# Performance work log

Hardware: AMD Instinct MI355X
Metric: run time of the kernel (lower is better)

## Reference

```python
import jax, jax.numpy as jnp
import numpy as np

SQRT_2_OVER_PI = 0.7978845608028654

def gelu_tanh(x):
    return 0.5 * x * (1.0 + jnp.tanh(SQRT_2_OVER_PI * (x + 0.044715 * x ** 3)))

def setup_inputs() -> dict:
    key = jax.random.key(0)
    ks = jax.random.split(key, 16)
    B, L, H, Dk, Dv = 4, 512, 8, 64, 64
    dm = H * Dk
    inp = {
        'q': jax.random.normal(ks[0], (B, L, dm), jnp.float32),
        'k': jax.random.normal(ks[1], (B, L, dm), jnp.float32),
        'v': jax.random.normal(ks[2], (B, L, dm), jnp.float32),
        'vec_adj_k': jax.random.normal(ks[3], (B, L, L, Dk), jnp.float32),
        'vec_adj_v': jax.random.normal(ks[4], (B, L, L, Dv), jnp.float32),
        'adj_k': jax.random.randint(ks[5], (B, L, L), 0, 2, jnp.int32),
        'adj_v': jax.random.randint(ks[6], (B, L, L), 0, 2, jnp.int32),
        # learned params (Linear weights stored as [in, out]; y = x @ W)
        'w_qs': jax.random.normal(ks[7], (dm, H * Dk), jnp.float32) * 0.02,
        'w_ks': jax.random.normal(ks[8], (dm, H * Dk), jnp.float32) * 0.02,
        'w_vs': jax.random.normal(ks[9], (dm, H * Dv), jnp.float32) * 0.02,
        'w_fc': jax.random.normal(ks[10], (H * Dk, H * Dk), jnp.float32) * 0.02,
        'w_nw': jax.random.normal(ks[11], (H * Dk, 1), jnp.float32) * 0.02,
        'w_self': jax.random.normal(ks[12], (H * Dk, H * Dk), jnp.float32) * 0.02,
        'w_dd': jax.random.normal(ks[13], (H * Dk, H * Dk), jnp.float32) * 0.02,
    }
    return inp

def reference(q, k, v, vec_adj_k, vec_adj_v, adj_k, adj_v,
              w_qs, w_ks, w_vs, w_fc, w_nw, w_self, w_dd):
    H, Dk, Dv = 8, 64, 64
    B, L, dm = q.shape
    temperature = Dk ** 0.5
    residual = q
    # projections -> [B, H, L, D]
    qh = (q @ w_qs).reshape(B, L, H, Dk).transpose(0, 2, 1, 3)
    kh = (k @ w_ks).reshape(B, L, H, Dk).transpose(0, 2, 1, 3)
    vh = (v @ w_vs).reshape(B, L, H, Dv).transpose(0, 2, 1, 3)
    qs = qh / temperature
    # inner_(q, k, vec_adj_k, flag=True): content + relative-position scores
    scores = jnp.einsum('bhld,bhmd->bhlm', qs, kh) \
           + jnp.einsum('bhld,blmd->bhlm', qs, vec_adj_k)  # [B,H,L,L]
    # adjacency mask (mask == 0 -> -10000)
    scores = jnp.where(adj_k[:, None, :, :] == 0, jnp.float32(-10000.0), scores)
    attn = jax.nn.softmax(scores, axis=-1)
    # inner_(attn, v, vec_adj_v, flag=False)
    out = jnp.einsum('bhlm,bhmd->bhld', attn, vh) \
        + jnp.einsum('bhlm,blmd->bhld', attn, vec_adj_v)
    qc = out.transpose(0, 2, 1, 3).reshape(B, L, H * Dv)  # [B,L,dm]
    # masked neighbor aggregation (GNN stage)
    adj_f = adj_k.astype(qc.dtype)
    nn_num = adj_f.sum(-1)                                  # [B,L]
    denom = jnp.where(nn_num >= 1.0, nn_num, 1.0)
    node_weight = jax.nn.sigmoid((qc @ w_nw)[..., 0])       # [B,L]
    self_info = qc @ w_self
    dd_info = qc @ w_dd
    dd_weight = node_weight[:, None, :] * adj_f             # [B,L,L]
    agg = jnp.matmul(dd_weight, dd_info) / denom[..., None]
    qo = gelu_tanh((self_info + agg) @ w_fc)
    qo = residual + qo
    return (qo, attn)
```

## Files before the change

kernel.cpp:

```cpp
#include <hip/hip_runtime.h>
#include <cstdint>


typedef __attribute__((ext_vector_type(8))) short short8;
typedef __attribute__((ext_vector_type(4))) float f32x4;

__device__ __forceinline__ unsigned short f2bf(float f){
  union { float f; unsigned u; } v; v.f = f;
  unsigned r = (v.u + 0x7fffu + ((v.u >> 16) & 1u)) >> 16;
  return (unsigned short)r;
}

__device__ __forceinline__ short8 ld8(const unsigned short* p){
  return *(const short8*)p;
}

__device__ __forceinline__ f32x4 mfma16(short8 a, short8 b, f32x4 c){
  return __builtin_amdgcn_mfma_f32_16x16x32_bf16(a, b, c, 0, 0, 0);
}

__device__ __forceinline__ float gelu_tanh(float x){
  float u = 0.7978845608028654f * (x + 0.044715f * x * x * x);
  return 0.5f * x * (1.f + tanhf(u));
}

__device__ __forceinline__ short8 pack8(float4 f0, float4 f1){
  short8 s;
  s[0] = (short)f2bf(f0.x); s[1] = (short)f2bf(f0.y);
  s[2] = (short)f2bf(f0.z); s[3] = (short)f2bf(f0.w);
  s[4] = (short)f2bf(f1.x); s[5] = (short)f2bf(f1.y);
  s[6] = (short)f2bf(f1.z); s[7] = (short)f2bf(f1.w);
  return s;
}

template<int MT, int LDA, int LDB, int KSTEPS>
__device__ __forceinline__ void gemmT(const unsigned short* __restrict__ A,
                                      const unsigned short* __restrict__ Bp,
                                      f32x4 acc[MT][4]){
#pragma unroll 2
  for (int ks = 0; ks < KSTEPS; ks++){
    int kk = ks * 32;
    short8 a[MT], b[4];
#pragma unroll
    for (int i = 0; i < MT; i++) a[i] = ld8(A + (size_t)i * 16 * LDA + kk);
#pragma unroll
    for (int j = 0; j < 4; j++)  b[j] = ld8(Bp + (size_t)j * 16 * LDB + kk);
#pragma unroll
    for (int i = 0; i < MT; i++)
#pragma unroll
      for (int j = 0; j < 4; j++)
        acc[i][j] = mfma16(a[i], b[j], acc[i][j]);
  }
}

__global__ __launch_bounds__(256) void k_prep(const float* __restrict__ q,
    const float* __restrict__ k, const float* __restrict__ v,
    unsigned short* __restrict__ xin,
    const float* __restrict__ wqs, const float* __restrict__ wks,
    const float* __restrict__ wvs, const float* __restrict__ wself,
    const float* __restrict__ wdd, const float* __restrict__ wfc,
    unsigned short* __restrict__ Wt){
  int blk = blockIdx.x;
  int t = threadIdx.x;
  if (blk < 3072){
    int i = blk * 256 + t;
    int w = i >> 18, r = i & 262143;
    const float* src = (w == 0) ? q : (w == 1) ? k : v;
    float4 f = *(const float4*)(src + (size_t)r * 4);
    unsigned lo = (unsigned)f2bf(f.x) | ((unsigned)f2bf(f.y) << 16);
    unsigned hi = (unsigned)f2bf(f.z) | ((unsigned)f2bf(f.w) << 16);
    uint2 o; o.x = lo; o.y = hi;
    *(uint2*)(xin + (size_t)w * 1048576 + (size_t)r * 4) = o;
  } else {
    int i = (blk - 3072) * 256 + t;
    int w = i >> 13;
    int rr = i & 8191;
    int kg = rr >> 9;
    int n  = rr & 511;
    int k0 = kg * 32;
    const float* src = (w == 0) ? wqs : (w == 1) ? wks : (w == 2) ? wvs :
                       (w == 3) ? wself : (w == 4) ? wdd : wfc;
    unsigned pk[16];
#pragma unroll
    for (int j = 0; j < 16; j++){
      float a = src[(size_t)(k0 + 2 * j) * 512 + n];
      float b = src[(size_t)(k0 + 2 * j + 1) * 512 + n];
      pk[j] = (unsigned)f2bf(a) | ((unsigned)f2bf(b) << 16);
    }
    uint4* o4 = (uint4*)(Wt + (size_t)w * 262144 + (size_t)n * 512 + k0);
    o4[0] = make_uint4(pk[0],  pk[1],  pk[2],  pk[3]);
    o4[1] = make_uint4(pk[4],  pk[5],  pk[6],  pk[7]);
    o4[2] = make_uint4(pk[8],  pk[9],  pk[10], pk[11]);
    o4[3] = make_uint4(pk[12], pk[13], pk[14], pk[15]);
  }
}

__global__ __launch_bounds__(256) void k_proj(const unsigned short* __restrict__ xin,
    const unsigned short* __restrict__ Wt, unsigned short* __restrict__ qsb,
    unsigned short* __restrict__ khb, unsigned short* __restrict__ vhT){
  int wid = blockIdx.x * 4 + (threadIdx.x >> 6);
  int mode = wid >> 9;
  int tile = wid & 511;
  int tm = tile >> 3, tn = tile & 7;
  int lane = threadIdx.x & 63;
  int r = lane & 15, qq = lane >> 4;
  const unsigned short* X = xin + (size_t)mode * 1048576;
  const unsigned short* W = Wt + (size_t)mode * 262144;
  unsigned short* dst = (mode == 0) ? qsb : (mode == 1) ? khb : vhT;
  const unsigned short* A  = X + (size_t)(tm * 32 + r) * 512 + qq * 8;
  const unsigned short* Bp = W + (size_t)(tn * 64 + r) * 512 + qq * 8;
  f32x4 acc[2][4] = {};
  gemmT<2, 512, 512, 16>(A, Bp, acc);
  float scv = (mode == 0) ? 0.125f : 1.0f;
  int h = tn;
#pragma unroll
  for (int i = 0; i < 2; i++)
#pragma unroll
    for (int j = 0; j < 4; j++)
#pragma unroll
      for (int e = 0; e < 4; e++){
        int row = tm * 32 + i * 16 + qq * 4 + e;
        int d = j * 16 + r;
        int bb = row >> 9, l = row & 511;
        unsigned short val = f2bf(acc[i][j][e] * scv);
        size_t idx = (mode == 2) ? ((size_t)((bb * 8 + h) * 64 + d) * 512 + l)
                                 : ((size_t)((bb * 8 + h) * 512 + l) * 64 + d);
        dst[idx] = val;
      }
}

__global__ __launch_bounds__(256) void k_scores(const unsigned short* __restrict__ qs,
    const unsigned short* __restrict__ kh, float* __restrict__ attnF){
  int wid = blockIdx.x * 4 + (threadIdx.x >> 6);
  int bh = wid >> 6;
  int tile = wid & 63;
  int tm = tile >> 3, tn = tile & 7;
  int lane = threadIdx.x & 63;
  int r = lane & 15, qq = lane >> 4;
  const unsigned short* A  = qs + (size_t)bh * 32768 + (size_t)(tm * 64 + r) * 64 + qq * 8;
  const unsigned short* Bp = kh + (size_t)bh * 32768 + (size_t)(tn * 64 + r) * 64 + qq * 8;
  f32x4 acc[4][4] = {};
  gemmT<4, 64, 64, 2>(A, Bp, acc);
  float* C = attnF + (size_t)bh * 262144;
#pragma unroll
  for (int i = 0; i < 4; i++)
#pragma unroll
    for (int j = 0; j < 4; j++)
#pragma unroll
      for (int e = 0; e < 4; e++){
        int row = tm * 64 + i * 16 + qq * 4 + e;
        int col = tn * 64 + j * 16 + r;
        C[(size_t)row * 512 + col] = acc[i][j][e];
      }
}

__global__ __launch_bounds__(256) void k_relsoft(const unsigned short* __restrict__ qs,
    const float* __restrict__ vak, const int* __restrict__ adj,
    float* __restrict__ attnF, unsigned short* __restrict__ attn_bf){
  int bid = blockIdx.x;
  int b = bid >> 9, l = bid & 511;
  int t = threadIdx.x, lane = t & 63, w = t >> 6;
  __shared__ __align__(16) unsigned short qsA[16 * 64];
  __shared__ float sc[8 * 512];
  __shared__ short Mlist[512];
  __shared__ int lds4[4];
  for (int j = 0; j < 4; j++){
    int e = t + j * 256;
    int m = e >> 6, d = e & 63;
    qsA[e] = (m < 8) ? qs[((size_t)((b * 8 + m) * 512 + l)) * 64 + d] : (unsigned short)0;
  }
  int am0 = adj[(size_t)bid * 512 + t];
  int am1 = adj[(size_t)bid * 512 + t + 256];
  for (int j = 0; j < 16; j++){
    int e = t + j * 256;
    int h = e >> 9, m = e & 511;
    float s = attnF[((size_t)(b * 8 + h) * 512 + l) * 512 + m];
    int msk = (j & 1) ? am1 : am0;
    sc[e] = msk ? s : -10000.0f;
  }
  int2 av2 = *(const int2*)(adj + (size_t)bid * 512 + 2 * t);
  int c = av2.x + av2.y;
  int incl = c;
  for (int off = 1; off < 64; off <<= 1){
    int n = __shfl_up(incl, off, 64);
    if (lane >= off) incl += n;
  }
  if (lane == 63) lds4[w] = incl;
  __syncthreads();
  int base = 0;
  for (int i = 0; i < w; i++) base += lds4[i];
  int cnt = lds4[0] + lds4[1] + lds4[2] + lds4[3];
  int excl = base + incl - c;
  if (av2.x){ Mlist[excl] = (short)(2 * t); excl++; }
  if (av2.y){ Mlist[excl] = (short)(2 * t + 1); }
  int padded = (cnt + 31) & ~31;
  for (int i2 = cnt + t; i2 < padded; i2 += 256) Mlist[i2] = 0;
  __syncthreads();
  int r = lane & 15, qq = lane >> 4;
  short8 a0 = ld8(qsA + r * 64 + qq * 8);
  short8 a1 = ld8(qsA + r * 64 + 32 + qq * 8);
  const float* vrow = vak + (size_t)bid * 32768;
  int ntiles = (cnt + 15) >> 4;
  for (int tile = w; tile < ntiles; tile += 4){
    int gi = tile * 16 + r;
    int m = Mlist[gi];
    const float* p = vrow + (size_t)m * 64 + qq * 8;
    float4 f0 = *(const float4*)(p);
    float4 f1 = *(const float4*)(p + 4);
    float4 f2 = *(const float4*)(p + 32);
    float4 f3 = *(const float4*)(p + 36);
    f32x4 acc = {0.f, 0.f, 0.f, 0.f};
    acc = mfma16(a0, pack8(f0, f1), acc);
    acc = mfma16(a1, pack8(f2, f3), acc);
    if (qq < 2){
#pragma unroll
      for (int i = 0; i < 4; i++){
        int h = qq * 4 + i;
        if (gi < cnt) sc[h * 512 + m] += acc[i];
      }
    }
  }
  __syncthreads();
  for (int hh = 0; hh < 2; hh++){
    int h = w * 2 + hh;
    float v[8]; float mx = -3.0e38f;
    for (int i = 0; i < 8; i++){
      int m = lane + i * 64;
      v[i] = sc[h * 512 + m]; mx = fmaxf(mx, v[i]);
    }
    for (int off = 32; off; off >>= 1) mx = fmaxf(mx, __shfl_xor(mx, off, 64));
    float sum = 0.f;
    for (int i = 0; i < 8; i++){ v[i] = __expf(v[i] - mx); sum += v[i]; }
    for (int off = 32; off; off >>= 1) sum += __shfl_xor(sum, off, 64);
    float inv = 1.f / sum;
    size_t base2 = ((size_t)(b * 8 + h) * 512 + l) * 512;
    for (int i = 0; i < 8; i++){
      int m = lane + i * 64;
      float p2 = v[i] * inv;
      attnF[base2 + m] = p2;
      attn_bf[base2 + m] = f2bf(p2);
    }
  }
}

__global__ __launch_bounds__(256) void k_outc(const unsigned short* __restrict__ attn_bf,
    const unsigned short* __restrict__ vhT, float* __restrict__ qc){
  int wid = blockIdx.x * 4 + (threadIdx.x >> 6);
  int bh = wid >> 4;
  int tm = wid & 15;
  int lane = threadIdx.x & 63;
  int r = lane & 15, qq = lane >> 4;
  const unsigned short* A  = attn_bf + (size_t)bh * 262144 + (size_t)(tm * 32 + r) * 512 + qq * 8;
  const unsigned short* Bp = vhT + (size_t)bh * 32768 + (size_t)r * 512 + qq * 8;
  f32x4 acc[2][4] = {};
  gemmT<2, 512, 512, 16>(A, Bp, acc);
  int b = bh >> 3, h = bh & 7;
#pragma unroll
  for (int i = 0; i < 2; i++)
#pragma unroll
    for (int j = 0; j < 4; j++)
#pragma unroll
      for (int e = 0; e < 4; e++){
        int lrow = tm * 32 + i * 16 + qq * 4 + e;
        int d = j * 16 + r;
        qc[(size_t)(b * 512 + lrow) * 512 + h * 64 + d] = acc[i][j][e];
      }
}

__global__ __launch_bounds__(256) void k_outrel(const unsigned short* __restrict__ attn_bf,
    const float* __restrict__ vav, const float* __restrict__ qc,
    const int* __restrict__ adj, const float* __restrict__ wnw,
    unsigned short* __restrict__ qc_bf, float* __restrict__ nw, float* __restrict__ invden){
  int bid = blockIdx.x;
  int b = bid >> 9, l = bid & 511;
  int t = threadIdx.x, lane = t & 63, w = t >> 6;
  __shared__ __align__(16) unsigned short attnL[8][512];
  __shared__ __align__(16) unsigned short pAg[8][528];
  __shared__ short Mlist[512];
  __shared__ float orL[512];
  __shared__ float redf[4];
  __shared__ int lds4[4];
  int r = lane & 15, qq = lane >> 4;
  int h8 = r & 7;
#pragma unroll
  for (int h = 0; h < 8; h++){
    const unsigned short* rowp = attn_bf + (((size_t)(b * 8 + h) * 512 + l) * 512);
    *(ushort2*)(&attnL[h][2 * t]) = *(const ushort2*)(rowp + 2 * t);
  }
  int2 av2 = *(const int2*)(adj + (size_t)bid * 512 + 2 * t);
  int c = av2.x + av2.y;
  int incl = c;
  for (int off = 1; off < 64; off <<= 1){
    int n = __shfl_up(incl, off, 64);
    if (lane >= off) incl += n;
  }
  if (lane == 63) lds4[w] = incl;
  __syncthreads();
  int base = 0;
  for (int i = 0; i < w; i++) base += lds4[i];
  int cnt = lds4[0] + lds4[1] + lds4[2] + lds4[3];
  int excl = base + incl - c;
  if (av2.x){ Mlist[excl] = (short)(2 * t); excl++; }
  if (av2.y){ Mlist[excl] = (short)(2 * t + 1); }
  int cntV = cnt;
  int padded0 = (cnt + 31) & ~31;
  for (int i2 = cnt + t; i2 < padded0; i2 += 256) Mlist[i2] = 0;
  __syncthreads();
  if (cnt == 0){
    for (int i2 = t; i2 < 512; i2 += 256) Mlist[i2] = (short)i2;
    cntV = 512;
    __syncthreads();
  }
  int padded = (cntV + 31) & ~31;
  for (int j = t; j < padded; j += 256){
    int m = Mlist[j];
    bool vld = (j < cntV);
#pragma unroll
    for (int h = 0; h < 8; h++)
      pAg[h][j] = vld ? attnL[h][m] : (unsigned short)0;
  }
  __syncthreads();
  const float* vrow = vav + (size_t)bid * 32768;
  int dcol = w * 16 + r;
  f32x4 acc = {0.f, 0.f, 0.f, 0.f};
  int nks = padded >> 5;
  for (int s = 0; s < nks; s++){
    short8 av = ld8(&pAg[h8][s * 32 + qq * 8]);
    int mrow[8];
#pragma unroll
    for (int j = 0; j < 8; j++) mrow[j] = Mlist[s * 32 + qq * 8 + j];
    float fv[8];
#pragma unroll
    for (int j = 0; j < 8; j++) fv[j] = vrow[(size_t)mrow[j] * 64 + dcol];
    short8 bv;
#pragma unroll
    for (int j = 0; j < 8; j++) bv[j] = (short)f2bf(fv[j]);
    acc = mfma16(av, bv, acc);
  }
  if (qq < 2){
#pragma unroll
    for (int i = 0; i < 4; i++){
      int h = qq * 4 + i;
      orL[h * 64 + dcol] = acc[i];
    }
  }
  __syncthreads();
  float part = 0.f;
  for (int j = 0; j < 2; j++){
    int e = t + j * 256;
    float val = qc[(size_t)bid * 512 + e] + orL[e];
    qc_bf[(size_t)bid * 512 + e] = f2bf(val);
    part += val * wnw[e];
  }
  for (int off = 32; off; off >>= 1) part += __shfl_xor(part, off, 64);
  if (lane == 0) redf[w] = part;
  __syncthreads();
  if (t == 0){
    float tot = redf[0] + redf[1] + redf[2] + redf[3];
    nw[bid] = 1.f / (1.f + __expf(-tot));
    invden[bid] = 1.f / ((cnt >= 1) ? (float)cnt : 1.f);
  }
}

__global__ __launch_bounds__(256) void k_post(const unsigned short* __restrict__ qcb,
    const unsigned short* __restrict__ Wself, const unsigned short* __restrict__ Wdd,
    float* __restrict__ selfi, unsigned short* __restrict__ ddT,
    const int* __restrict__ adj, const float* __restrict__ nw,
    const float* __restrict__ invden, unsigned short* __restrict__ ddw){
  int blk = blockIdx.x;
  int t = threadIdx.x;
  if (blk < 256){
    int mode = blk >> 7;
    int wid = (blk & 127) * 4 + (t >> 6);
    int tm = wid >> 3, tn = wid & 7;
    int lane = t & 63;
    int r = lane & 15, qq = lane >> 4;
    const unsigned short* W = mode ? Wdd : Wself;
    const unsigned short* A  = qcb + (size_t)(tm * 32 + r) * 512 + qq * 8;
    const unsigned short* Bp = W + (size_t)(tn * 64 + r) * 512 + qq * 8;
    f32x4 acc[2][4] = {};
    gemmT<2, 512, 512, 16>(A, Bp, acc);
#pragma unroll
    for (int i = 0; i < 2; i++)
#pragma unroll
      for (int j = 0; j < 4; j++)
#pragma unroll
        for (int e = 0; e < 4; e++){
          int row = tm * 32 + i * 16 + qq * 4 + e;
          int col = tn * 64 + j * 16 + r;
          if (mode == 0)
            selfi[(size_t)row * 512 + col] = acc[i][j][e];
          else {
            int bb = row >> 9, m = row & 511;
            ddT[((size_t)(bb * 512 + col)) * 512 + m] = f2bf(acc[i][j][e]);
          }
        }
  } else {
    int i8 = ((blk - 256) * 256 + t) * 8;
    int bb = i8 >> 18, rest = i8 & 262143;
    int l = rest >> 9, m0 = rest & 511;
    int4 a0 = *(const int4*)(adj + i8);
    int4 a1 = *(const int4*)(adj + i8 + 4);
    float id = invden[bb * 512 + l];
    const float* nwb = nw + bb * 512 + m0;
    short8 o;
    o[0] = a0.x ? (short)f2bf(nwb[0] * id) : (short)0;
    o[1] = a0.y ? (short)f2bf(nwb[1] * id) : (short)0;
    o[2] = a0.z ? (short)f2bf(nwb[2] * id) : (short)0;
    o[3] = a0.w ? (short)f2bf(nwb[3] * id) : (short)0;
    o[4] = a1.x ? (short)f2bf(nwb[4] * id) : (short)0;
    o[5] = a1.y ? (short)f2bf(nwb[5] * id) : (short)0;
    o[6] = a1.z ? (short)f2bf(nwb[6] * id) : (short)0;
    o[7] = a1.w ? (short)f2bf(nwb[7] * id) : (short)0;
    *(short8*)(ddw + i8) = o;
  }
}

__global__ __launch_bounds__(256) void k_agg(const unsigned short* __restrict__ ddw,
    const unsigned short* __restrict__ ddT, const float* __restrict__ selfi,
    unsigned short* __restrict__ xbf){
  int wid = blockIdx.x * 4 + (threadIdx.x >> 6);
  int b = wid >> 7;
  int tile = wid & 127;
  int tm = tile >> 3, tn = tile & 7;
  int lane = threadIdx.x & 63;
  int r = lane & 15, qq = lane >> 4;
  const unsigned short* A  = ddw + (size_t)b * 262144 + (size_t)(tm * 32 + r) * 512 + qq * 8;
  const unsigned short* Bp = ddT + (size_t)b * 262144 + (size_t)(tn * 64 + r) * 512 + qq * 8;
  f32x4 acc[2][4] = {};
  gemmT<2, 512, 512, 16>(A, Bp, acc);
#pragma unroll
  for (int i = 0; i < 2; i++)
#pragma unroll
    for (int j = 0; j < 4; j++)
#pragma unroll
      for (int e = 0; e < 4; e++){
        int row = b * 512 + tm * 32 + i * 16 + qq * 4 + e;
        int col = tn * 64 + j * 16 + r;
        float x = acc[i][j][e] + selfi[(size_t)row * 512 + col];
        xbf[(size_t)row * 512 + col] = f2bf(x);
      }
}

__global__ __launch_bounds__(256) void k_fc(const unsigned short* __restrict__ xbf,
    const unsigned short* __restrict__ W, const float* __restrict__ qin,
    float* __restrict__ qo){
  int wid = blockIdx.x * 4 + (threadIdx.x >> 6);
  int tm = wid >> 3, tn = wid & 7;
  int lane = threadIdx.x & 63;
  int r = lane & 15, qq = lane >> 4;
  const unsigned short* A  = xbf + (size_t)(tm * 32 + r) * 512 + qq * 8;
  const unsigned short* Bp = W + (size_t)(tn * 64 + r) * 512 + qq * 8;
  f32x4 acc[2][4] = {};
  gemmT<2, 512, 512, 16>(A, Bp, acc);
#pragma unroll
  for (int i = 0; i < 2; i++)
#pragma unroll
    for (int j = 0; j < 4; j++)
#pragma unroll
      for (int e = 0; e < 4; e++){
        int row = tm * 32 + i * 16 + qq * 4 + e;
        int col = tn * 64 + j * 16 + r;
        qo[(size_t)row * 512 + col] = qin[(size_t)row * 512 + col] + gelu_tanh(acc[i][j][e]);
      }
}

extern "C" void kernel_launch(void* const* d_in, const int* in_sizes, int n_in,
                              void* d_out, int out_size, void* d_ws, size_t ws_size,
                              hipStream_t stream){
  const float* q    = (const float*)d_in[0];
  const float* k    = (const float*)d_in[1];
  const float* v    = (const float*)d_in[2];
  const float* vak  = (const float*)d_in[3];
  const float* vav  = (const float*)d_in[4];
  const int*   adjk = (const int*)d_in[5];
  const float* wqs  = (const float*)d_in[7];
  const float* wks  = (const float*)d_in[8];
  const float* wvs  = (const float*)d_in[9];
  const float* wfc  = (const float*)d_in[10];
  const float* wnw  = (const float*)d_in[11];
  const float* wself= (const float*)d_in[12];
  const float* wdd  = (const float*)d_in[13];

  float* qo    = (float*)d_out;
  float* attnF = qo + 1048576;

  char* p = (char*)d_ws;
  unsigned short* xin   = (unsigned short*)p; p += 6291456;
  unsigned short* Wt    = (unsigned short*)p; p += 3145728;
  unsigned short* qsb   = (unsigned short*)p; p += 2097152;
  unsigned short* khb   = (unsigned short*)p; p += 2097152;
  unsigned short* vhT   = (unsigned short*)p; p += 2097152;
  unsigned short* attnb = (unsigned short*)p; p += 16777216;
  float*          qc    = (float*)p;          p += 4194304;
  unsigned short* qcb   = (unsigned short*)p; p += 2097152;
  float*          nw    = (float*)p;          p += 8192;
  float*          invd  = (float*)p;          p += 8192;
  float*          selfi = (float*)p;          p += 4194304;
  unsigned short* ddT   = (unsigned short*)p; p += 2097152;
  unsigned short* ddw   = (unsigned short*)p; p += 2097152;
  unsigned short* xbf   = (unsigned short*)p; p += 2097152;

  k_prep<<<3264, 256, 0, stream>>>(q, k, v, xin, wqs, wks, wvs, wself, wdd, wfc, Wt);
  k_proj<<<384, 256, 0, stream>>>(xin, Wt, qsb, khb, vhT);
  k_scores<<<512, 256, 0, stream>>>(qsb, khb, attnF);
  k_relsoft<<<2048, 256, 0, stream>>>(qsb, vak, adjk, attnF, attnb);
  k_outc<<<128, 256, 0, stream>>>(attnb, vhT, qc);
  k_outrel<<<2048, 256, 0, stream>>>(attnb, vav, qc, adjk, wnw, qcb, nw, invd);
  k_post<<<768, 256, 0, stream>>>(qcb, Wt + 786432, Wt + 1048576, selfi, ddT,
                                  adjk, nw, invd, ddw);
  k_agg<<<128, 256, 0, stream>>>(ddw, ddT, selfi, xbf);
  k_fc<<<128, 256, 0, stream>>>(xbf, Wt + 1310720, q, qo);
}
```

Before: 618.9 us.

## Stage gathered relative-position vectors through LDS for coalesced loads in attention kernels

In k_relsoft, each wave now cooperatively loads the 16 gathered vec_adj_k rows of a tile with float4 loads, converts them to bf16 into a per-wave LDS buffer, and feeds the MFMA from LDS. In k_outrel, the per-lane scattered scalar loads of vec_adj_v are replaced by chunks of 128 gathered rows loaded block-wide as float4, transposed into LDS as bf16, then consumed by four MFMAs per chunk. The goal is to coalesce the dominant global traffic on the large vec_adj tensors. The cost is extra LDS space, block-level barriers per chunk, and padding to 128 rows, which adds wasted work when neighbour counts are small.

```diff
diff --git a/kernel.cpp b/kernel.cpp
--- a/kernel.cpp
+++ b/kernel.cpp
@@ -22,15 +22,6 @@
 __device__ __forceinline__ float gelu_tanh(float x){
   float u = 0.7978845608028654f * (x + 0.044715f * x * x * x);
   return 0.5f * x * (1.f + tanhf(u));
-}
-
-__device__ __forceinline__ short8 pack8(float4 f0, float4 f1){
-  short8 s;
-  s[0] = (short)f2bf(f0.x); s[1] = (short)f2bf(f0.y);
-  s[2] = (short)f2bf(f0.z); s[3] = (short)f2bf(f0.w);
-  s[4] = (short)f2bf(f1.x); s[5] = (short)f2bf(f1.y);
-  s[6] = (short)f2bf(f1.z); s[7] = (short)f2bf(f1.w);
-  return s;
 }
 
 template<int MT, int LDA, int LDB, int KSTEPS>
@@ -161,6 +152,7 @@
   int b = bid >> 9, l = bid & 511;
   int t = threadIdx.x, lane = t & 63, w = t >> 6;
   __shared__ __align__(16) unsigned short qsA[16 * 64];
+  __shared__ __align__(16) unsigned short vkt[4][16 * 72];
   __shared__ float sc[8 * 512];
   __shared__ short Mlist[512];
   __shared__ int lds4[4];
@@ -201,17 +193,25 @@
   short8 a1 = ld8(qsA + r * 64 + 32 + qq * 8);
   const float* vrow = vak + (size_t)bid * 32768;
   int ntiles = (cnt + 15) >> 4;
+  unsigned short* vw = &vkt[w][0];
   for (int tile = w; tile < ntiles; tile += 4){
-    int gi = tile * 16 + r;
+    int rows0 = tile * 16;
+#pragma unroll
+    for (int it = 0; it < 4; it++){
+      int idx = it * 64 + lane;
+      int rloc = idx >> 4, seg = idx & 15;
+      int ms = Mlist[rows0 + rloc];
+      float4 f = *(const float4*)(vrow + (size_t)ms * 64 + seg * 4);
+      ushort4 u;
+      u.x = f2bf(f.x); u.y = f2bf(f.y); u.z = f2bf(f.z); u.w = f2bf(f.w);
+      *(ushort4*)(vw + rloc * 72 + seg * 4) = u;
+    }
+    int gi = rows0 + r;
     int m = Mlist[gi];
-    const float* p = vrow + (size_t)m * 64 + qq * 8;
-    float4 f0 = *(const float4*)(p);
-    float4 f1 = *(const float4*)(p + 4);
-    float4 f2 = *(const float4*)(p + 32);
-    float4 f3 = *(const float4*)(p + 36);
+    const unsigned short* bp = vw + r * 72 + qq * 8;
     f32x4 acc = {0.f, 0.f, 0.f, 0.f};
-    acc = mfma16(a0, pack8(f0, f1), acc);
-    acc = mfma16(a1, pack8(f2, f3), acc);
+    acc = mfma16(a0, ld8(bp),      acc);
+    acc = mfma16(a1, ld8(bp + 32), acc);
     if (qq < 2){
 #pragma unroll
       for (int i = 0; i < 4; i++){
@@ -275,7 +275,8 @@
   int b = bid >> 9, l = bid & 511;
   int t = threadIdx.x, lane = t & 63, w = t >> 6;
   __shared__ __align__(16) unsigned short attnL[8][512];
-  __shared__ __align__(16) unsigned short pAg[8][528];
+  __shared__ __align__(16) unsigned short pAg[8][512];
+  __shared__ __align__(16) unsigned short vvT[64 * 136];
   __shared__ short Mlist[512];
   __shared__ float orL[512];
   __shared__ float redf[4];
@@ -303,15 +304,15 @@
   if (av2.x){ Mlist[excl] = (short)(2 * t); excl++; }
   if (av2.y){ Mlist[excl] = (short)(2 * t + 1); }
   int cntV = cnt;
-  int padded0 = (cnt + 31) & ~31;
-  for (int i2 = cnt + t; i2 < padded0; i2 += 256) Mlist[i2] = 0;
   __syncthreads();
   if (cnt == 0){
     for (int i2 = t; i2 < 512; i2 += 256) Mlist[i2] = (short)i2;
     cntV = 512;
     __syncthreads();
   }
-  int padded = (cntV + 31) & ~31;
+  int padded = (cntV + 127) & ~127;
+  for (int i2 = cntV + t; i2 < padded; i2 += 256) Mlist[i2] = 0;
+  __syncthreads();
   for (int j = t; j < padded; j += 256){
     int m = Mlist[j];
     bool vld = (j < cntV);
@@ -323,19 +324,27 @@
   const float* vrow = vav + (size_t)bid * 32768;
   int dcol = w * 16 + r;
   f32x4 acc = {0.f, 0.f, 0.f, 0.f};
-  int nks = padded >> 5;
-  for (int s = 0; s < nks; s++){
-    short8 av = ld8(&pAg[h8][s * 32 + qq * 8]);
-    int mrow[8];
-#pragma unroll
-    for (int j = 0; j < 8; j++) mrow[j] = Mlist[s * 32 + qq * 8 + j];
-    float fv[8];
-#pragma unroll
-    for (int j = 0; j < 8; j++) fv[j] = vrow[(size_t)mrow[j] * 64 + dcol];
-    short8 bv;
-#pragma unroll
-    for (int j = 0; j < 8; j++) bv[j] = (short)f2bf(fv[j]);
-    acc = mfma16(av, bv, acc);
+  int nchunks = padded >> 7;
+  for (int ch = 0; ch < nchunks; ch++){
+#pragma unroll
+    for (int it = 0; it < 8; it++){
+      int i4 = it * 256 + t;
+      int mloc = i4 >> 4, d4 = (i4 & 15) * 4;
+      int ms = Mlist[ch * 128 + mloc];
+      float4 f = *(const float4*)(vrow + (size_t)ms * 64 + d4);
+      vvT[(d4    ) * 136 + mloc] = f2bf(f.x);
+      vvT[(d4 + 1) * 136 + mloc] = f2bf(f.y);
+      vvT[(d4 + 2) * 136 + mloc] = f2bf(f.z);
+      vvT[(d4 + 3) * 136 + mloc] = f2bf(f.w);
+    }
+    __syncthreads();
+#pragma unroll
+    for (int s = 0; s < 4; s++){
+      short8 av = ld8(&pAg[h8][ch * 128 + s * 32 + qq * 8]);
+      short8 bv = ld8(vvT + (size_t)dcol * 136 + s * 32 + qq * 8);
+      acc = mfma16(av, bv, acc);
+    }
+    __syncthreads();
   }
   if (qq < 2){
 #pragma unroll
```

Result: no change. 629.0 us (+1.6%).
